# Kernel tuning notes

Hardware: AMD Instinct MI355X
Metric: run time of the kernel (lower is better)

The kernel has to match this reference:

```python
import jax, jax.numpy as jnp
import numpy as np

N_HEAD = 16
ROT_DIM = 64  # partial rotary dims (< head_size=128)


def _apply_rope(x, cos, sin):
    # x: [B,H,T,R]; cos/sin: [T,R/2]. LLaMA-style pairwise complex rotation.
    x1 = x[..., 0::2]
    x2 = x[..., 1::2]
    c = cos[None, None, :, :]
    s = sin[None, None, :, :]
    o1 = x1 * c - x2 * s
    o2 = x1 * s + x2 * c
    # interleave back: [..., R/2, 2] -> [..., R]
    out = jnp.stack([o1, o2], axis=-1)
    return out.reshape(x.shape)


def setup_inputs() -> dict:
    key = jax.random.key(0)
    k1, k2, k3 = jax.random.split(key, 3)
    B, T, C = 2, 2048, 2048
    D = C // N_HEAD
    x = jax.random.normal(k1, (B, T, C), dtype=jnp.float32)
    W_attn = jax.random.normal(k2, (C, 3 * C), dtype=jnp.float32) * (1.0 / np.sqrt(C))
    W_proj = jax.random.normal(k3, (C, C), dtype=jnp.float32) * (1.0 / np.sqrt(C))
    # rotary cos/sin tables over ROT_DIM dims
    half = ROT_DIM // 2
    inv_freq = 1.0 / (10000.0 ** (np.arange(0, half, dtype=np.float32) / half))
    t = np.arange(T, dtype=np.float32)
    ang = np.outer(t, inv_freq)  # [T, R/2]
    cos = jnp.asarray(np.cos(ang), dtype=jnp.float32)
    sin = jnp.asarray(np.sin(ang), dtype=jnp.float32)
    return {"x": x, "W_attn": W_attn, "W_proj": W_proj, "cos": cos, "sin": sin}


def reference(x, W_attn, W_proj, cos, sin):
    B, T, C = x.shape
    H = N_HEAD
    D = C // H
    qkv = x @ W_attn  # [B,T,3C]
    q, k, v = jnp.split(qkv, 3, axis=-1)
    # [B,T,C] -> [B,H,T,D]
    q = q.reshape(B, T, H, D).transpose(0, 2, 1, 3)
    k = k.reshape(B, T, H, D).transpose(0, 2, 1, 3)
    v = v.reshape(B, T, H, D).transpose(0, 2, 1, 3)
    # partial RoPE on first ROT_DIM dims
    q = jnp.concatenate([_apply_rope(q[..., :ROT_DIM], cos, sin), q[..., ROT_DIM:]], axis=-1)
    k = jnp.concatenate([_apply_rope(k[..., :ROT_DIM], cos, sin), k[..., ROT_DIM:]], axis=-1)
    # bidirectional SDPA, no mask
    scale = 1.0 / jnp.sqrt(jnp.asarray(D, dtype=x.dtype))
    scores = jnp.einsum("bhqd,bhkd->bhqk", q, k) * scale
    attn = jax.nn.softmax(scores, axis=-1)
    y = jnp.einsum("bhqk,bhkd->bhqd", attn, v)  # [B,H,T,D]
    y = y.transpose(0, 2, 1, 3).reshape(B, T, C)
    return y @ W_proj
```

## Files before the change

### kernel.cpp

```cpp
#include <hip/hip_runtime.h>
#include <stdint.h>

typedef unsigned short u16;
typedef __attribute__((ext_vector_type(8))) short short8;
typedef __attribute__((ext_vector_type(4))) float f32x4;

__device__ __forceinline__ float bf2f(u16 u){
  union { uint32_t i; float f; } v; v.i = ((uint32_t)u) << 16; return v.f;
}
__device__ __forceinline__ u16 f2bf(float f){
  union { float f; uint32_t i; } v; v.f = f;
  uint32_t r = v.i + 0x7FFFu + ((v.i >> 16) & 1u);
  return (u16)(r >> 16);
}

typedef __attribute__((address_space(3))) uint32_t lds_u32;
typedef const __attribute__((address_space(1))) uint32_t gl_u32;
__device__ __forceinline__ void gl_lds16(const void* g, void* lds){
  __builtin_amdgcn_global_load_lds((gl_u32*)g, (lds_u32*)lds, 16, 0, 0);
}

__global__ void cast_f32_bf16(const float* __restrict__ src, u16* __restrict__ dst){
  const int i = blockIdx.x * 256 + threadIdx.x;
  const float4 a = ((const float4*)src)[2 * i];
  const float4 b = ((const float4*)src)[2 * i + 1];
  uint4 o;
  o.x = (uint32_t)f2bf(a.x) | ((uint32_t)f2bf(a.y) << 16);
  o.y = (uint32_t)f2bf(a.z) | ((uint32_t)f2bf(a.w) << 16);
  o.z = (uint32_t)f2bf(b.x) | ((uint32_t)f2bf(b.y) << 16);
  o.w = (uint32_t)f2bf(b.z) | ((uint32_t)f2bf(b.w) << 16);
  ((uint4*)dst)[i] = o;
}

__global__ void transpose_f32_bf16(const float* __restrict__ src, u16* __restrict__ dst,
                                   int R, int C){
  __shared__ u16 tile[32][33];
  const int cb = blockIdx.x * 32, rb = blockIdx.y * 32;
  const int tx = threadIdx.x, ty = threadIdx.y;
  #pragma unroll
  for (int i = 0; i < 32; i += 8)
    tile[ty + i][tx] = f2bf(src[(size_t)(rb + ty + i) * C + cb + tx]);
  __syncthreads();
  #pragma unroll
  for (int i = 0; i < 32; i += 8)
    dst[(size_t)(cb + ty + i) * R + rb + tx] = tile[tx][ty + i];
}

__global__ void transpose_v(const u16* __restrict__ qkv, u16* __restrict__ vT){
  __shared__ u16 tile[32][33];
  const int db = blockIdx.x * 32, tb = blockIdx.y * 32, bh = blockIdx.z;
  const int b = bh >> 4, h = bh & 15;
  const int tx = threadIdx.x, ty = threadIdx.y;
  const u16* src = qkv + (size_t)(b * 2048) * 6144 + 4096 + h * 128;
  #pragma unroll
  for (int i = 0; i < 32; i += 8) tile[ty + i][tx] = src[(size_t)(tb + ty + i) * 6144 + db + tx];
  __syncthreads();
  u16* d = vT + (size_t)bh * 128 * 2048;
  #pragma unroll
  for (int i = 0; i < 32; i += 8) d[(size_t)(db + ty + i) * 2048 + tb + tx] = tile[tx][ty + i];
}

__global__ void rope_qk(const u16* __restrict__ qkv, const float* __restrict__ cosb,
                        const float* __restrict__ sinb, u16* __restrict__ qo,
                        u16* __restrict__ ko){
  const int idx = blockIdx.x * 256 + threadIdx.x;
  const int d2 = idx & 63;
  const int h  = (idx >> 6) & 15;
  const int t  = (idx >> 10) & 2047;
  const int b  = (idx >> 21) & 1;
  const int w  = idx >> 22;
  const int incol = w * 2048 + h * 128 + 2 * d2;
  const uint32_t pair = *(const uint32_t*)(qkv + (size_t)(b * 2048 + t) * 6144 + incol);
  float x1 = bf2f((u16)(pair & 0xffff));
  float x2 = bf2f((u16)(pair >> 16));
  float o1 = x1, o2 = x2;
  if (d2 < 32){
    const float c = cosb[t * 32 + d2];
    const float s = sinb[t * 32 + d2];
    o1 = x1 * c - x2 * s;
    o2 = x1 * s + x2 * c;
  }
  const uint32_t outp = (uint32_t)f2bf(o1) | ((uint32_t)f2bf(o2) << 16);
  u16* dst = w ? ko : qo;
  *(uint32_t*)(dst + ((size_t)(b * 16 + h) * 2048 + t) * 128 + 2 * d2) = outp;
}

template<bool F32OUT>
__global__ __launch_bounds__(256) void gemm_bt(const u16* __restrict__ A,
                                               const u16* __restrict__ Bt,
                                               void* __restrict__ Cv,
                                               int M, int N, int K){
  __shared__ __align__(16) u16 sA[128 * 64];
  __shared__ __align__(16) u16 sB[128 * 64];
  const int tid  = threadIdx.x;
  const int lane = tid & 63, wave = tid >> 6;
  const int quad = lane >> 4, l15 = lane & 15;
  const int wr = wave >> 1, wc = wave & 1;
  const int mb = blockIdx.y * 128, nb = blockIdx.x * 128;

  f32x4 acc[4][4];
  #pragma unroll
  for (int i = 0; i < 4; i++)
    #pragma unroll
    for (int j = 0; j < 4; j++) acc[i][j] = (f32x4)0.0f;

  for (int k0 = 0; k0 < K; k0 += 64){
    const u16* Ab = A + (size_t)mb * K + k0;
    const u16* Bb = Bt + (size_t)nb * K + k0;
    #pragma unroll
    for (int r = 0; r < 4; r++){
      const int idx = r * 256 + tid;
      const int row = idx >> 3, c = idx & 7;
      const int gc = (c ^ (row & 7)) * 8;
      gl_lds16(Ab + (size_t)row * K + gc, (char*)sA + r * 4096 + wave * 1024);
      gl_lds16(Bb + (size_t)row * K + gc, (char*)sB + r * 4096 + wave * 1024);
    }
    __syncthreads();
    #pragma unroll
    for (int ks = 0; ks < 2; ks++){
      short8 af[4], bfr[4];
      #pragma unroll
      for (int i = 0; i < 4; i++){
        const int row = wr * 64 + i * 16 + l15;
        const int ch = (ks * 4 + quad) ^ (l15 & 7);
        af[i] = *(const short8*)((const char*)sA + row * 128 + ch * 16);
      }
      #pragma unroll
      for (int j = 0; j < 4; j++){
        const int row = wc * 64 + j * 16 + l15;
        const int ch = (ks * 4 + quad) ^ (l15 & 7);
        bfr[j] = *(const short8*)((const char*)sB + row * 128 + ch * 16);
      }
      #pragma unroll
      for (int i = 0; i < 4; i++)
        #pragma unroll
        for (int j = 0; j < 4; j++)
          acc[i][j] = __builtin_amdgcn_mfma_f32_16x16x32_bf16(af[i], bfr[j], acc[i][j], 0, 0, 0);
    }
    __syncthreads();
  }
  #pragma unroll
  for (int i = 0; i < 4; i++)
    #pragma unroll
    for (int j = 0; j < 4; j++)
      #pragma unroll
      for (int r = 0; r < 4; r++){
        const int row = mb + wr * 64 + i * 16 + quad * 4 + r;
        const int col = nb + wc * 64 + j * 16 + l15;
        if (F32OUT) ((float*)Cv)[(size_t)row * N + col] = acc[i][j][r];
        else        ((u16*)Cv)[(size_t)row * N + col]   = f2bf(acc[i][j][r]);
      }
}

__device__ __forceinline__ void stage8k(const u16* __restrict__ g, int ldK,
                                        char* lds, int call, int tid){
  const int idx = call * 512 + tid;
  const int row = idx >> 3, c = idx & 7;
  gl_lds16(g + (size_t)row * ldK + ((c ^ (row & 7)) * 8),
           lds + call * 8192 + (tid >> 6) * 1024);
}

template<bool F32OUT>
__global__ __launch_bounds__(512, 2) void gemm256_bt(const u16* __restrict__ A,
                                                     const u16* __restrict__ Bt,
                                                     void* __restrict__ Cv,
                                                     int M, int N, int K){
  __shared__ __align__(16) u16 sA[2 * 256 * 64];
  __shared__ __align__(16) u16 sB[2 * 256 * 64];
  const int tid  = threadIdx.x;
  const int lane = tid & 63, wave = tid >> 6;
  const int quad = lane >> 4, l15 = lane & 15;
  const int wm = wave >> 2, wn = wave & 3;

  const int nx = gridDim.x, ny = gridDim.y;
  const int bid = blockIdx.y * nx + blockIdx.x;
  int row, col;
  if ((nx & 7) == 0){
    const int xcd = bid & 7, c = bid >> 3;
    const int cq = c / ny;
    col = xcd * (nx >> 3) + cq;
    row = c - cq * ny;
  } else { col = bid % nx; row = bid / nx; }
  const int mb = row * 256, nb = col * 256;

  const int NT = K >> 6;
  const u16* Ab = A  + (size_t)mb * K;
  const u16* Bb = Bt + (size_t)nb * K;

  f32x4 acc[8][4];
  #pragma unroll
  for (int i = 0; i < 8; i++)
    #pragma unroll
    for (int n = 0; n < 4; n++) acc[i][n] = (f32x4)0.0f;

  #pragma unroll
  for (int r = 0; r < 4; r++) stage8k(Ab, K, (char*)sA, r, tid);
  #pragma unroll
  for (int r = 0; r < 4; r++) stage8k(Bb, K, (char*)sB, r, tid);
  #pragma unroll
  for (int r = 0; r < 4; r++) stage8k(Bb + 64, K, (char*)sB + 32768, r, tid);
  asm volatile("s_waitcnt vmcnt(4)" ::: "memory");
  __builtin_amdgcn_s_barrier();

  for (int s = 0; s < NT; ++s){
    const int cur = s & 1;
    char* sAc = (char*)sA + cur * 32768;
    char* sBc = (char*)sB + cur * 32768;
    char* sAn = (char*)sA + (cur ^ 1) * 32768;
    const u16* An = Ab + (size_t)(s + 1) * 64;
    const u16* Bn = Bb + (size_t)(s + 2) * 64;
    const bool pfA = (s + 1 < NT), pfB = (s + 2 < NT);

    short8 bq[4][2];
    #pragma unroll
    for (int q = 0; q < 4; q++){
      if (q == 0){
        #pragma unroll
        for (int n = 0; n < 4; n++)
          #pragma unroll
          for (int ks = 0; ks < 2; ks++){
            const int row2 = wn * 64 + n * 16 + l15;
            bq[n][ks] = *(const short8*)(sBc + row2 * 128 +
                                         (((ks * 4 + quad) ^ (l15 & 7)) * 16));
          }
      }
      short8 aq[2][2];
      #pragma unroll
      for (int i = 0; i < 2; i++)
        #pragma unroll
        for (int ks = 0; ks < 2; ks++){
          const int row2 = wm * 128 + (q * 2 + i) * 16 + l15;
          aq[i][ks] = *(const short8*)(sAc + row2 * 128 +
                                       (((ks * 4 + quad) ^ (l15 & 7)) * 16));
        }
      if (q == 0 && pfA){ stage8k(An, K, sAn, 0, tid); stage8k(An, K, sAn, 1, tid); }
      if (q == 1 && pfA){ stage8k(An, K, sAn, 2, tid); stage8k(An, K, sAn, 3, tid); }
      if (q == 2 && pfB){ stage8k(Bn, K, sBc, 0, tid); stage8k(Bn, K, sBc, 1, tid); }
      if (q == 3 && pfB){ stage8k(Bn, K, sBc, 2, tid); stage8k(Bn, K, sBc, 3, tid); }

      __builtin_amdgcn_s_barrier();
      asm volatile("s_waitcnt lgkmcnt(0)" ::: "memory");
      __builtin_amdgcn_s_setprio(1);
      #pragma unroll
      for (int ks = 0; ks < 2; ks++)
        #pragma unroll
        for (int i = 0; i < 2; i++)
          #pragma unroll
          for (int n = 0; n < 4; n++)
            acc[q * 2 + i][n] = __builtin_amdgcn_mfma_f32_16x16x32_bf16(
                aq[i][ks], bq[n][ks], acc[q * 2 + i][n], 0, 0, 0);
      __builtin_amdgcn_s_setprio(0);
      if (q == 3){
        if (pfB)      asm volatile("s_waitcnt vmcnt(4)" ::: "memory");
        else if (pfA) asm volatile("s_waitcnt vmcnt(0)" ::: "memory");
      }
      __builtin_amdgcn_s_barrier();
    }
  }

  #pragma unroll
  for (int i = 0; i < 8; i++)
    #pragma unroll
    for (int n = 0; n < 4; n++)
      #pragma unroll
      for (int r = 0; r < 4; r++){
        const int row2 = mb + wm * 128 + i * 16 + quad * 4 + r;
        const int col2 = nb + wn * 64 + n * 16 + l15;
        if (F32OUT) ((float*)Cv)[(size_t)row2 * N + col2] = acc[i][n][r];
        else        ((u16*)Cv)[(size_t)row2 * N + col2]   = f2bf(acc[i][n][r]);
      }
}

__global__ __launch_bounds__(256, 4) void attn(const u16* __restrict__ q,
                                               const u16* __restrict__ k,
                                               const u16* __restrict__ vT,
                                               u16* __restrict__ y){
  __shared__ __align__(16) u16 bufK[64 * 128];
  __shared__ __align__(16) u16 bufV[128 * 64];
  __shared__ __align__(16) u16 bufP[4 * 16 * 64];
  const int tid  = threadIdx.x;
  const int lane = tid & 63, wave = tid >> 6;
  const int quad = lane >> 4, l15 = lane & 15;
  const int bh = blockIdx.x & 31, qt = blockIdx.x >> 5;
  const u16* qbh = q  + (size_t)bh * 2048 * 128;
  const u16* kbh = k  + (size_t)bh * 2048 * 128;
  const u16* vbh = vT + (size_t)bh * 128 * 2048;
  const float scale2 = 0.12754100060254310f;

  #pragma unroll
  for (int rr = 0; rr < 4; rr++){
    const int idx = rr * 256 + tid;
    const int row = idx >> 4, c = idx & 15;
    gl_lds16(qbh + (size_t)(qt * 64 + row) * 128 + ((c ^ (row & 15)) * 8),
             (char*)bufK + rr * 4096 + wave * 1024);
  }
  __syncthreads();
  short8 qf[4];
  #pragma unroll
  for (int ks = 0; ks < 4; ks++){
    const int row = wave * 16 + l15;
    const int ch = (ks * 4 + quad) ^ l15;
    qf[ks] = *(const short8*)((const char*)bufK + row * 256 + ch * 16);
  }
  __syncthreads();

  #pragma unroll
  for (int rr = 0; rr < 4; rr++){
    const int idx = rr * 256 + tid;
    const int row = idx >> 4, c = idx & 15;
    gl_lds16(kbh + (size_t)row * 128 + ((c ^ (row & 15)) * 8),
             (char*)bufK + rr * 4096 + wave * 1024);
  }
  __syncthreads();
  #pragma unroll
  for (int rr = 0; rr < 4; rr++){
    const int idx = rr * 256 + tid;
    const int row = idx >> 3, c = idx & 7;
    gl_lds16(vbh + (size_t)row * 2048 + ((c ^ (row & 7)) * 8),
             (char*)bufV + rr * 4096 + wave * 1024);
  }

  f32x4 o[8];
  #pragma unroll
  for (int ds = 0; ds < 8; ds++) o[ds] = (f32x4)0.0f;
  float l_[4] = {0.0f, 0.0f, 0.0f, 0.0f};

  for (int kt = 0; kt < 32; kt++){
    f32x4 s[4];
    #pragma unroll
    for (int kv = 0; kv < 4; kv++) s[kv] = (f32x4)0.0f;
    #pragma unroll
    for (int ks = 0; ks < 4; ks++){
      short8 bfr[4];
      #pragma unroll
      for (int kv = 0; kv < 4; kv++){
        const int row = kv * 16 + l15;
        const int ch = (ks * 4 + quad) ^ l15;
        bfr[kv] = *(const short8*)((const char*)bufK + row * 256 + ch * 16);
      }
      __builtin_amdgcn_s_setprio(1);
      #pragma unroll
      for (int kv = 0; kv < 4; kv++)
        s[kv] = __builtin_amdgcn_mfma_f32_16x16x32_bf16(qf[ks], bfr[kv], s[kv], 0, 0, 0);
      __builtin_amdgcn_s_setprio(0);
    }

    #pragma unroll
    for (int kv = 0; kv < 4; kv++)
      #pragma unroll
      for (int r = 0; r < 4; r++){
        const float p = exp2f(s[kv][r] * scale2);
        s[kv][r] = p;
        l_[r] += p;
      }

    __syncthreads();

    if (kt < 31){
      #pragma unroll
      for (int rr = 0; rr < 4; rr++){
        const int idx = rr * 256 + tid;
        const int row = idx >> 4, c = idx & 15;
        gl_lds16(kbh + (size_t)((kt + 1) * 64 + row) * 128 + ((c ^ (row & 15)) * 8),
                 (char*)bufK + rr * 4096 + wave * 1024);
      }
    }

    #pragma unroll
    for (int kv = 0; kv < 4; kv++)
      #pragma unroll
      for (int r = 0; r < 4; r++){
        const int row = quad * 4 + r;
        const int col = kv * 16 + l15;
        bufP[wave * 1024 + row * 64 + (((col >> 3) ^ (row & 7)) * 8) + (col & 7)]
          = f2bf(s[kv][r]);
      }

    #pragma unroll
    for (int ks = 0; ks < 2; ks++){
      const short8 pa = *(const short8*)((const char*)bufP + wave * 2048 +
                                         l15 * 128 + (((ks * 4 + quad) ^ (l15 & 7)) * 16));
      short8 vb[8];
      #pragma unroll
      for (int ds = 0; ds < 8; ds++){
        const int row = ds * 16 + l15;
        const int ch = (ks * 4 + quad) ^ (row & 7);
        vb[ds] = *(const short8*)((const char*)bufV + row * 128 + ch * 16);
      }
      __builtin_amdgcn_s_setprio(1);
      #pragma unroll
      for (int ds = 0; ds < 8; ds++)
        o[ds] = __builtin_amdgcn_mfma_f32_16x16x32_bf16(pa, vb[ds], o[ds], 0, 0, 0);
      __builtin_amdgcn_s_setprio(0);
    }

    __syncthreads();

    if (kt < 31){
      #pragma unroll
      for (int rr = 0; rr < 4; rr++){
        const int idx = rr * 256 + tid;
        const int row = idx >> 3, c = idx & 7;
        gl_lds16(vbh + (size_t)row * 2048 + (kt + 1) * 64 + ((c ^ (row & 7)) * 8),
                 (char*)bufV + rr * 4096 + wave * 1024);
      }
    }
  }

  #pragma unroll
  for (int r = 0; r < 4; r++){
    #pragma unroll
    for (int off = 1; off < 16; off <<= 1) l_[r] += __shfl_xor(l_[r], off);
  }

  const int b = bh >> 4, h = bh & 15;
  float inv[4];
  #pragma unroll
  for (int r = 0; r < 4; r++) inv[r] = 1.0f / l_[r];
  #pragma unroll
  for (int ds = 0; ds < 8; ds++)
    #pragma unroll
    for (int r = 0; r < 4; r++){
      const int t = qt * 64 + wave * 16 + quad * 4 + r;
      const int cc = h * 128 + ds * 16 + l15;
      y[((size_t)(b * 2048 + t)) * 2048 + cc] = f2bf(o[ds][r] * inv[r]);
    }
}

extern "C" void kernel_launch(void* const* d_in, const int* in_sizes, int n_in,
                              void* d_out, int out_size, void* d_ws, size_t ws_size,
                              hipStream_t stream) {
  const float* x    = (const float*)d_in[0];
  const float* Wa   = (const float*)d_in[1];
  const float* Wp   = (const float*)d_in[2];
  const float* cosb = (const float*)d_in[3];
  const float* sinb = (const float*)d_in[4];
  float* out = (float*)d_out;
  char* ws = (char*)d_ws;

  u16* WaT = (u16*)(ws);
  u16* WpT = (u16*)(ws + 25165824);
  u16* xb  = (u16*)(ws + 33554432);
  u16* qkv = (u16*)(ws + 50331648);
  u16* qb  = (u16*)(ws + 100663296);
  u16* kb  = (u16*)(ws + 117440512);
  u16* vTb = (u16*)(ws + 134217728);
  u16* yb  = (u16*)(ws + 33554432);

  dim3 b32(32, 8, 1);
  transpose_f32_bf16<<<dim3(192, 64, 1), b32, 0, stream>>>(Wa, WaT, 2048, 6144);
  transpose_f32_bf16<<<dim3(64, 64, 1),  b32, 0, stream>>>(Wp, WpT, 2048, 2048);
  cast_f32_bf16<<<4096, 256, 0, stream>>>(x, xb);
  gemm256_bt<false><<<dim3(24, 16, 1), 512, 0, stream>>>(xb, WaT, qkv, 4096, 6144, 2048);
  rope_qk<<<32768, 256, 0, stream>>>(qkv, cosb, sinb, qb, kb);
  transpose_v<<<dim3(4, 64, 32), b32, 0, stream>>>(qkv, vTb);
  attn<<<1024, 256, 0, stream>>>(qb, kb, vTb, yb);
  gemm_bt<true><<<dim3(16, 32, 1), 256, 0, stream>>>(yb, WpT, out, 4096, 2048, 2048);
}
```

Before: 447.8 us.

## Process 32 query rows per wave in attention to reuse K/V tiles

Each attention wave now handles two 16-row query sub-tiles, so a workgroup covers 128 queries and each K/V tile loaded into LDS is shared by twice as many MFMAs. The grid is halved to 512 blocks and launch bounds are lowered to 2 waves per SIMD to make room for the doubled accumulators. The setprio hints are also removed. The aim is to cut K/V global traffic and LDS reads per FLOP, at the cost of fewer blocks in flight and more register pressure.

```diff
diff --git a/kernel.cpp b/kernel.cpp
--- a/kernel.cpp
+++ b/kernel.cpp
@@ -271,13 +271,13 @@
       }
 }
 
-__global__ __launch_bounds__(256, 4) void attn(const u16* __restrict__ q,
+__global__ __launch_bounds__(256, 2) void attn(const u16* __restrict__ q,
                                                const u16* __restrict__ k,
                                                const u16* __restrict__ vT,
                                                u16* __restrict__ y){
   __shared__ __align__(16) u16 bufK[64 * 128];
   __shared__ __align__(16) u16 bufV[128 * 64];
-  __shared__ __align__(16) u16 bufP[4 * 16 * 64];
+  __shared__ __align__(16) u16 bufP[4 * 32 * 64];
   const int tid  = threadIdx.x;
   const int lane = tid & 63, wave = tid >> 6;
   const int quad = lane >> 4, l15 = lane & 15;
@@ -287,22 +287,30 @@
   const u16* vbh = vT + (size_t)bh * 128 * 2048;
   const float scale2 = 0.12754100060254310f;
 
-  #pragma unroll
-  for (int rr = 0; rr < 4; rr++){
-    const int idx = rr * 256 + tid;
-    const int row = idx >> 4, c = idx & 15;
-    gl_lds16(qbh + (size_t)(qt * 64 + row) * 128 + ((c ^ (row & 15)) * 8),
-             (char*)bufK + rr * 4096 + wave * 1024);
-  }
-  __syncthreads();
-  short8 qf[4];
-  #pragma unroll
-  for (int ks = 0; ks < 4; ks++){
-    const int row = wave * 16 + l15;
-    const int ch = (ks * 4 + quad) ^ l15;
-    qf[ks] = *(const short8*)((const char*)bufK + row * 256 + ch * 16);
-  }
-  __syncthreads();
+  short8 qf[2][4];
+  #pragma unroll
+  for (int p = 0; p < 2; p++){
+    #pragma unroll
+    for (int rr = 0; rr < 4; rr++){
+      const int idx = rr * 256 + tid;
+      const int row = idx >> 4, c = idx & 15;
+      gl_lds16(qbh + (size_t)(qt * 128 + p * 64 + row) * 128 + ((c ^ (row & 15)) * 8),
+               (char*)bufK + rr * 4096 + wave * 1024);
+    }
+    __syncthreads();
+    if ((wave >> 1) == p){
+      const int rbase = (wave & 1) * 32;
+      #pragma unroll
+      for (int i = 0; i < 2; i++)
+        #pragma unroll
+        for (int ks = 0; ks < 4; ks++){
+          const int row = rbase + i * 16 + l15;
+          const int ch = (ks * 4 + quad) ^ l15;
+          qf[i][ks] = *(const short8*)((const char*)bufK + row * 256 + ch * 16);
+        }
+    }
+    __syncthreads();
+  }
 
   #pragma unroll
   for (int rr = 0; rr < 4; rr++){
@@ -320,15 +328,19 @@
              (char*)bufV + rr * 4096 + wave * 1024);
   }
 
-  f32x4 o[8];
-  #pragma unroll
-  for (int ds = 0; ds < 8; ds++) o[ds] = (f32x4)0.0f;
-  float l_[4] = {0.0f, 0.0f, 0.0f, 0.0f};
+  f32x4 o[2][8];
+  #pragma unroll
+  for (int i = 0; i < 2; i++)
+    #pragma unroll
+    for (int ds = 0; ds < 8; ds++) o[i][ds] = (f32x4)0.0f;
+  float l_[2][4] = {{0,0,0,0},{0,0,0,0}};
 
   for (int kt = 0; kt < 32; kt++){
-    f32x4 s[4];
-    #pragma unroll
-    for (int kv = 0; kv < 4; kv++) s[kv] = (f32x4)0.0f;
+    f32x4 s[2][4];
+    #pragma unroll
+    for (int i = 0; i < 2; i++)
+      #pragma unroll
+      for (int kv = 0; kv < 4; kv++) s[i][kv] = (f32x4)0.0f;
     #pragma unroll
     for (int ks = 0; ks < 4; ks++){
       short8 bfr[4];
@@ -338,21 +350,23 @@
         const int ch = (ks * 4 + quad) ^ l15;
         bfr[kv] = *(const short8*)((const char*)bufK + row * 256 + ch * 16);
       }
-      __builtin_amdgcn_s_setprio(1);
+      #pragma unroll
+      for (int i = 0; i < 2; i++)
+        #pragma unroll
+        for (int kv = 0; kv < 4; kv++)
+          s[i][kv] = __builtin_amdgcn_mfma_f32_16x16x32_bf16(qf[i][ks], bfr[kv], s[i][kv], 0, 0, 0);
+    }
+
+    #pragma unroll
+    for (int i = 0; i < 2; i++)
       #pragma unroll
       for (int kv = 0; kv < 4; kv++)
-        s[kv] = __builtin_amdgcn_mfma_f32_16x16x32_bf16(qf[ks], bfr[kv], s[kv], 0, 0, 0);
-      __builtin_amdgcn_s_setprio(0);
-    }
-
-    #pragma unroll
-    for (int kv = 0; kv < 4; kv++)
-      #pragma unroll
-      for (int r = 0; r < 4; r++){
-        const float p = exp2f(s[kv][r] * scale2);
-        s[kv][r] = p;
-        l_[r] += p;
-      }
+        #pragma unroll
+        for (int r = 0; r < 4; r++){
+          const float p = exp2f(s[i][kv][r] * scale2);
+          s[i][kv][r] = p;
+          l_[i][r] += p;
+        }
 
     __syncthreads();
 
@@ -367,19 +381,24 @@
     }
 
     #pragma unroll
-    for (int kv = 0; kv < 4; kv++)
-      #pragma unroll
-      for (int r = 0; r < 4; r++){
-        const int row = quad * 4 + r;
-        const int col = kv * 16 + l15;
-        bufP[wave * 1024 + row * 64 + (((col >> 3) ^ (row & 7)) * 8) + (col & 7)]
-          = f2bf(s[kv][r]);
-      }
+    for (int i = 0; i < 2; i++)
+      #pragma unroll
+      for (int kv = 0; kv < 4; kv++)
+        #pragma unroll
+        for (int r = 0; r < 4; r++){
+          const int row = i * 16 + quad * 4 + r;
+          const int col = kv * 16 + l15;
+          bufP[wave * 2048 + row * 64 + (((col >> 3) ^ (row & 7)) * 8) + (col & 7)]
+            = f2bf(s[i][kv][r]);
+        }
 
     #pragma unroll
     for (int ks = 0; ks < 2; ks++){
-      const short8 pa = *(const short8*)((const char*)bufP + wave * 2048 +
-                                         l15 * 128 + (((ks * 4 + quad) ^ (l15 & 7)) * 16));
+      short8 pa[2];
+      #pragma unroll
+      for (int i = 0; i < 2; i++)
+        pa[i] = *(const short8*)((const char*)bufP + wave * 4096 + (i * 16 + l15) * 128 +
+                                 (((ks * 4 + quad) ^ (l15 & 7)) * 16));
       short8 vb[8];
       #pragma unroll
       for (int ds = 0; ds < 8; ds++){
@@ -387,11 +406,11 @@
         const int ch = (ks * 4 + quad) ^ (row & 7);
         vb[ds] = *(const short8*)((const char*)bufV + row * 128 + ch * 16);
       }
-      __builtin_amdgcn_s_setprio(1);
       #pragma unroll
       for (int ds = 0; ds < 8; ds++)
-        o[ds] = __builtin_amdgcn_mfma_f32_16x16x32_bf16(pa, vb[ds], o[ds], 0, 0, 0);
-      __builtin_amdgcn_s_setprio(0);
+        #pragma unroll
+        for (int i = 0; i < 2; i++)
+          o[i][ds] = __builtin_amdgcn_mfma_f32_16x16x32_bf16(pa[i], vb[ds], o[i][ds], 0, 0, 0);
     }
 
     __syncthreads();
@@ -408,23 +427,29 @@
   }
 
   #pragma unroll
-  for (int r = 0; r < 4; r++){
-    #pragma unroll
-    for (int off = 1; off < 16; off <<= 1) l_[r] += __shfl_xor(l_[r], off);
-  }
+  for (int i = 0; i < 2; i++)
+    #pragma unroll
+    for (int r = 0; r < 4; r++){
+      #pragma unroll
+      for (int off = 1; off < 16; off <<= 1) l_[i][r] += __shfl_xor(l_[i][r], off);
+    }
 
   const int b = bh >> 4, h = bh & 15;
-  float inv[4];
-  #pragma unroll
-  for (int r = 0; r < 4; r++) inv[r] = 1.0f / l_[r];
-  #pragma unroll
-  for (int ds = 0; ds < 8; ds++)
-    #pragma unroll
-    for (int r = 0; r < 4; r++){
-      const int t = qt * 64 + wave * 16 + quad * 4 + r;
-      const int cc = h * 128 + ds * 16 + l15;
-      y[((size_t)(b * 2048 + t)) * 2048 + cc] = f2bf(o[ds][r] * inv[r]);
-    }
+  float inv[2][4];
+  #pragma unroll
+  for (int i = 0; i < 2; i++)
+    #pragma unroll
+    for (int r = 0; r < 4; r++) inv[i][r] = 1.0f / l_[i][r];
+  #pragma unroll
+  for (int i = 0; i < 2; i++)
+    #pragma unroll
+    for (int ds = 0; ds < 8; ds++)
+      #pragma unroll
+      for (int r = 0; r < 4; r++){
+        const int t = qt * 128 + wave * 32 + i * 16 + quad * 4 + r;
+        const int cc = h * 128 + ds * 16 + l15;
+        y[((size_t)(b * 2048 + t)) * 2048 + cc] = f2bf(o[i][ds][r] * inv[i][r]);
+      }
 }
 
 extern "C" void kernel_launch(void* const* d_in, const int* in_sizes, int n_in,
@@ -454,6 +479,6 @@
   gemm256_bt<false><<<dim3(24, 16, 1), 512, 0, stream>>>(xb, WaT, qkv, 4096, 6144, 2048);
   rope_qk<<<32768, 256, 0, stream>>>(qkv, cosb, sinb, qb, kb);
   transpose_v<<<dim3(4, 64, 32), b32, 0, stream>>>(qkv, vTb);
-  attn<<<1024, 256, 0, stream>>>(qb, kb, vTb, yb);
+  attn<<<512, 256, 0, stream>>>(qb, kb, vTb, yb);
   gemm_bt<true><<<dim3(16, 32, 1), 256, 0, stream>>>(yb, WpT, out, 4096, 2048, 2048);
 }
```

Result: faster. 422.0 us (-5.8%).
